# Optimization experiments

Hardware: AMD Instinct MI355X
Metric: run time of the kernel (lower is better)

Reference implementation:

```python
import jax, jax.numpy as jnp
import numpy as np

B, N, D, H = 64, 2048, 512, 512
CA, CB = 3, 5  # num classes per node type
EPS = 1e-5


def setup_inputs() -> dict:
    key = jax.random.key(0)
    ks = jax.random.split(key, 8)
    s = 1.0 / np.sqrt(D)
    x = jax.random.normal(ks[0], (B, N, D), dtype=jnp.float32)
    W1 = jax.random.uniform(ks[1], (D, H), jnp.float32, -s, s)
    b1 = jax.random.uniform(ks[2], (H,), jnp.float32, -s, s)
    gamma = jnp.ones((H,), jnp.float32)
    beta = jnp.zeros((H,), jnp.float32)
    sh = 1.0 / np.sqrt(H)
    Wa = jax.random.uniform(ks[3], (H, CA), jnp.float32, -sh, sh)
    ba = jax.random.uniform(ks[4], (CA,), jnp.float32, -sh, sh)
    Wb = jax.random.uniform(ks[5], (H, CB), jnp.float32, -sh, sh)
    bb = jax.random.uniform(ks[6], (CB,), jnp.float32, -sh, sh)
    idx_a = jnp.arange(0, N // 2, dtype=jnp.int64 if jax.config.jax_enable_x64 else jnp.int32)
    idx_b = jnp.arange(N // 2, N, dtype=idx_a.dtype)
    return {"x": x, "W1": W1, "b1": b1, "gamma": gamma, "beta": beta,
            "Wa": Wa, "ba": ba, "Wb": Wb, "bb": bb, "idx_a": idx_a, "idx_b": idx_b}


def reference(x, W1, b1, gamma, beta, Wa, ba, Wb, bb, idx_a, idx_b):
    # MLP block: Linear -> BatchNorm1d (training stats) -> ReLU on flattened rows
    h = x.reshape(-1, x.shape[-1]) @ W1 + b1            # [B*N, H]
    mu = h.mean(axis=0)
    var = h.var(axis=0)                                  # biased var, as BatchNorm1d normalization
    h = (h - mu) * jax.lax.rsqrt(var + EPS) * gamma + beta
    h = jax.nn.relu(h).reshape(x.shape[0], x.shape[1], -1)  # [B, N, H]

    out = jnp.zeros((x.shape[0], x.shape[1], 1), dtype=jnp.float32)
    for idx, W, b in ((idx_a, Wa, ba), (idx_b, Wb, bb)):
        logits = jnp.einsum('bnh,hc->bnc', h[:, idx, :], W) + b
        probs = jax.nn.softmax(logits, axis=-1)
        pred = jnp.argmax(probs, axis=-1, keepdims=True).astype(jnp.float32)
        out = out.at[:, idx, :].set(pred)
    return out
```

## Files before the change

kernel.cpp:

```cpp
#include <hip/hip_runtime.h>
#include <math.h>

constexpr int Bc = 64, Nc = 2048, Dc = 512, Hc = 512;
constexpr long long Mc = (long long)Bc * Nc;
constexpr int BM = 128, BN = 128, BK = 16;
constexpr int LDT = 132;

__global__ __launch_bounds__(256) void gemm_bias(const float* __restrict__ X,
                                                 const float* __restrict__ W,
                                                 const float* __restrict__ bias,
                                                 float* __restrict__ Hout)
{
    __shared__ float As[BK][LDT];
    __shared__ float Bs[BK][LDT];

    const int tid = threadIdx.x;
    const int bn = blockIdx.x;
    const int bm = blockIdx.y;
    const int m0 = bm * BM, n0 = bn * BN;

    const int wave = tid >> 6, lane = tid & 63;
    const int wm = wave >> 1, wn = wave & 1;
    const int lm = lane >> 3, ln = lane & 7;
    const int am = wm * 64 + lm * 8;
    const int an = wn * 64 + ln * 8;

    const int ar0 = tid >> 2;
    const int ak0 = (tid & 3) * 4;
    const int br0 = tid >> 5;
    const int bq0 = (tid & 31) * 4;

    const float* aBase = X + (size_t)(m0 + ar0) * Dc + ak0;
    const float* bBase = W + (size_t)br0 * Hc + n0 + bq0;

    float acc[8][8];
#pragma unroll
    for (int i = 0; i < 8; ++i)
#pragma unroll
        for (int j = 0; j < 8; ++j) acc[i][j] = 0.0f;

    float4 av0 = *(const float4*)(aBase);
    float4 av1 = *(const float4*)(aBase + (size_t)64 * Dc);
    float4 bv0 = *(const float4*)(bBase);
    float4 bv1 = *(const float4*)(bBase + (size_t)8 * Hc);

    for (int kt = 0; kt < Dc; kt += BK) {
        __syncthreads();
        As[ak0 + 0][ar0] = av0.x;  As[ak0 + 1][ar0] = av0.y;
        As[ak0 + 2][ar0] = av0.z;  As[ak0 + 3][ar0] = av0.w;
        As[ak0 + 0][ar0 + 64] = av1.x;  As[ak0 + 1][ar0 + 64] = av1.y;
        As[ak0 + 2][ar0 + 64] = av1.z;  As[ak0 + 3][ar0 + 64] = av1.w;
        *(float4*)&Bs[br0][bq0]     = bv0;
        *(float4*)&Bs[br0 + 8][bq0] = bv1;
        __syncthreads();

        const int kn = kt + BK;
        if (kn < Dc) {
            av0 = *(const float4*)(aBase + kn);
            av1 = *(const float4*)(aBase + (size_t)64 * Dc + kn);
            bv0 = *(const float4*)(bBase + (size_t)kn * Hc);
            bv1 = *(const float4*)(bBase + (size_t)(kn + 8) * Hc);
        }

#pragma unroll
        for (int k = 0; k < BK; ++k) {
            float4 a0 = *(const float4*)&As[k][am];
            float4 a1 = *(const float4*)&As[k][am + 4];
            float4 b0 = *(const float4*)&Bs[k][an];
            float4 b1 = *(const float4*)&Bs[k][an + 4];
            float a_[8] = {a0.x, a0.y, a0.z, a0.w, a1.x, a1.y, a1.z, a1.w};
            float b_[8] = {b0.x, b0.y, b0.z, b0.w, b1.x, b1.y, b1.z, b1.w};
#pragma unroll
            for (int i = 0; i < 8; ++i)
#pragma unroll
                for (int j = 0; j < 8; ++j)
                    acc[i][j] = fmaf(a_[i], b_[j], acc[i][j]);
        }
    }

    float4 c0 = *(const float4*)&bias[n0 + an];
    float4 c1 = *(const float4*)&bias[n0 + an + 4];
#pragma unroll
    for (int i = 0; i < 8; ++i) {
        const size_t row = (size_t)(m0 + am + i);
        float4 o0, o1;
        o0.x = acc[i][0] + c0.x; o0.y = acc[i][1] + c0.y;
        o0.z = acc[i][2] + c0.z; o0.w = acc[i][3] + c0.w;
        o1.x = acc[i][4] + c1.x; o1.y = acc[i][5] + c1.y;
        o1.z = acc[i][6] + c1.z; o1.w = acc[i][7] + c1.w;
        *(float4*)&Hout[row * Hc + n0 + an]     = o0;
        *(float4*)&Hout[row * Hc + n0 + an + 4] = o1;
    }
}

__global__ __launch_bounds__(256) void zero_stats(double* __restrict__ s)
{
    int i = blockIdx.x * 256 + threadIdx.x;
    if (i < 1024) s[i] = 0.0;
}

__global__ __launch_bounds__(256) void colstats(const float* __restrict__ Hbuf,
                                                double* __restrict__ sum,
                                                double* __restrict__ sumsq)
{
    const int c = threadIdx.x;
    const long long r0 = (long long)blockIdx.x * 256;
    float s0 = 0.f, q0 = 0.f, s1 = 0.f, q1 = 0.f;
    for (long long r = r0; r < r0 + 256; ++r) {
        float v0 = Hbuf[(size_t)r * Hc + c];
        float v1 = Hbuf[(size_t)r * Hc + c + 256];
        s0 += v0; q0 = fmaf(v0, v0, q0);
        s1 += v1; q1 = fmaf(v1, v1, q1);
    }
    atomicAdd(&sum[c], (double)s0);
    atomicAdd(&sumsq[c], (double)q0);
    atomicAdd(&sum[c + 256], (double)s1);
    atomicAdd(&sumsq[c + 256], (double)q1);
}

__global__ __launch_bounds__(256) void finalize_stats(const double* __restrict__ sum,
                                                      const double* __restrict__ sumsq,
                                                      const float* __restrict__ gamma,
                                                      const float* __restrict__ beta,
                                                      float* __restrict__ scale,
                                                      float* __restrict__ shift)
{
    int c = blockIdx.x * 256 + threadIdx.x;
    if (c < Hc) {
        double mu  = sum[c] / (double)Mc;
        double var = sumsq[c] / (double)Mc - mu * mu;
        double rstd = 1.0 / sqrt(var + 1e-5);
        float a = (float)rstd * gamma[c];
        scale[c] = a;
        shift[c] = beta[c] - (float)mu * a;
    }
}

template <int C>
__global__ __launch_bounds__(256) void head_kernel(const float* __restrict__ Hbuf,
                                                   const float* __restrict__ scale,
                                                   const float* __restrict__ shift,
                                                   const float* __restrict__ W,
                                                   const float* __restrict__ bias,
                                                   const int* __restrict__ idx,
                                                   float* __restrict__ out)
{
    const long long wid = ((long long)blockIdx.x * blockDim.x + threadIdx.x) >> 6;
    const int lane = threadIdx.x & 63;
    if (wid >= (long long)Bc * (Nc / 2)) return;
    const int b   = (int)(wid >> 10);
    const int pos = (int)(wid & 1023);
    const int n   = idx[pos];
    const size_t row = (size_t)b * Nc + n;

    const int i0 = lane * 8;
    float4 h0 = *(const float4*)&Hbuf[row * Hc + i0];
    float4 h1 = *(const float4*)&Hbuf[row * Hc + i0 + 4];
    float4 s0 = *(const float4*)&scale[i0];
    float4 s1 = *(const float4*)&scale[i0 + 4];
    float4 t0 = *(const float4*)&shift[i0];
    float4 t1 = *(const float4*)&shift[i0 + 4];

    float v[8];
    v[0] = fmaxf(fmaf(h0.x, s0.x, t0.x), 0.f);
    v[1] = fmaxf(fmaf(h0.y, s0.y, t0.y), 0.f);
    v[2] = fmaxf(fmaf(h0.z, s0.z, t0.z), 0.f);
    v[3] = fmaxf(fmaf(h0.w, s0.w, t0.w), 0.f);
    v[4] = fmaxf(fmaf(h1.x, s1.x, t1.x), 0.f);
    v[5] = fmaxf(fmaf(h1.y, s1.y, t1.y), 0.f);
    v[6] = fmaxf(fmaf(h1.z, s1.z, t1.z), 0.f);
    v[7] = fmaxf(fmaf(h1.w, s1.w, t1.w), 0.f);

    float p[C];
#pragma unroll
    for (int c = 0; c < C; ++c) p[c] = 0.f;
#pragma unroll
    for (int u = 0; u < 8; ++u) {
        const float* wrow = W + (size_t)(i0 + u) * C;
#pragma unroll
        for (int c = 0; c < C; ++c) p[c] = fmaf(v[u], wrow[c], p[c]);
    }
#pragma unroll
    for (int off = 32; off; off >>= 1)
#pragma unroll
        for (int c = 0; c < C; ++c) p[c] += __shfl_xor(p[c], off);

    if (lane == 0) {
        float best = p[0] + bias[0];
        int bi = 0;
#pragma unroll
        for (int c = 1; c < C; ++c) {
            float l = p[c] + bias[c];
            if (l > best) { best = l; bi = c; }
        }
        out[row] = (float)bi;
    }
}

extern "C" void kernel_launch(void* const* d_in, const int* in_sizes, int n_in,
                              void* d_out, int out_size, void* d_ws, size_t ws_size,
                              hipStream_t stream)
{
    (void)in_sizes; (void)n_in; (void)out_size; (void)ws_size;
    const float* x     = (const float*)d_in[0];
    const float* W1    = (const float*)d_in[1];
    const float* b1    = (const float*)d_in[2];
    const float* gamma = (const float*)d_in[3];
    const float* beta  = (const float*)d_in[4];
    const float* Wa    = (const float*)d_in[5];
    const float* ba    = (const float*)d_in[6];
    const float* Wb    = (const float*)d_in[7];
    const float* bb    = (const float*)d_in[8];
    const int*   idx_a = (const int*)d_in[9];
    const int*   idx_b = (const int*)d_in[10];
    float* out = (float*)d_out;

    char* ws = (char*)d_ws;
    float*  Hbuf  = (float*)ws;
    double* sums  = (double*)(ws + (size_t)Mc * Hc * 4);
    float*  scale = (float*)((char*)sums + 1024 * sizeof(double));
    float*  shift = scale + Hc;

    zero_stats<<<4, 256, 0, stream>>>(sums);
    gemm_bias<<<dim3(4, 1024), 256, 0, stream>>>(x, W1, b1, Hbuf);
    colstats<<<512, 256, 0, stream>>>(Hbuf, sums, sums + 512);
    finalize_stats<<<2, 256, 0, stream>>>(sums, sums + 512, gamma, beta, scale, shift);

    const long long waves_half = (long long)Bc * (Nc / 2);
    const int blocks_half = (int)((waves_half * 64 + 255) / 256);
    head_kernel<3><<<blocks_half, 256, 0, stream>>>(Hbuf, scale, shift, Wa, ba, idx_a, out);
    head_kernel<5><<<blocks_half, 256, 0, stream>>>(Hbuf, scale, shift, Wb, bb, idx_b, out);
}
```

Baseline: 1.154 ms.

## Fuse column stats into GEMM epilogue, async-load W to LDS, merge head kernels

Folds the BatchNorm column sum and sum-of-squares reduction into the GEMM epilogue using wave shuffles, shared memory and double atomics. This removes the separate colstats pass, which reread the whole 256 MB H buffer. The GEMM now uses BK=32, loads W tiles straight into double-buffered LDS with global_load_lds, and maps workgroups to XCDs to improve L2 locality. The two head kernels become one launch, which cuts launch overhead at the cost of more LDS use and a more complex GEMM schedule.

```diff
diff --git a/kernel.cpp b/kernel.cpp
--- a/kernel.cpp
+++ b/kernel.cpp
@@ -3,35 +3,56 @@
 
 constexpr int Bc = 64, Nc = 2048, Dc = 512, Hc = 512;
 constexpr long long Mc = (long long)Bc * Nc;
-constexpr int BM = 128, BN = 128, BK = 16;
-constexpr int LDT = 132;
-
-__global__ __launch_bounds__(256) void gemm_bias(const float* __restrict__ X,
-                                                 const float* __restrict__ W,
-                                                 const float* __restrict__ bias,
-                                                 float* __restrict__ Hout)
-{
-    __shared__ float As[BK][LDT];
-    __shared__ float Bs[BK][LDT];
+constexpr int BM = 128, BN = 128, BK = 32;
+constexpr int LDA_ = 132;
+
+__device__ __forceinline__ void gload16(const float* g, void* lds) {
+    __builtin_amdgcn_global_load_lds(
+        (const __attribute__((address_space(1))) void*)g,
+        (__attribute__((address_space(3))) void*)lds, 16, 0, 0);
+}
+
+__global__ __launch_bounds__(256) void gemm_fused(const float* __restrict__ X,
+                                                  const float* __restrict__ W,
+                                                  const float* __restrict__ bias,
+                                                  float* __restrict__ Hout,
+                                                  double* __restrict__ stats )
+{
+    __shared__ float As[BK][LDA_];
+    __shared__ float Bs[2][BK][BN];
+    __shared__ float sred[4][128];
+
+    const int wgid = blockIdx.x;
+    const int xcd  = wgid & 7;
+    const int slot = wgid >> 3;
+    const int bm   = xcd * 128 + (slot >> 2);
+    const int bn   = slot & 3;
+    const int m0 = bm * BM, n0 = bn * BN;
 
     const int tid = threadIdx.x;
-    const int bn = blockIdx.x;
-    const int bm = blockIdx.y;
-    const int m0 = bm * BM, n0 = bn * BN;
-
     const int wave = tid >> 6, lane = tid & 63;
     const int wm = wave >> 1, wn = wave & 1;
     const int lm = lane >> 3, ln = lane & 7;
     const int am = wm * 64 + lm * 8;
     const int an = wn * 64 + ln * 8;
 
-    const int ar0 = tid >> 2;
-    const int ak0 = (tid & 3) * 4;
-    const int br0 = tid >> 5;
-    const int bq0 = (tid & 31) * 4;
-
-    const float* aBase = X + (size_t)(m0 + ar0) * Dc + ak0;
-    const float* bBase = W + (size_t)br0 * Hc + n0 + bq0;
+    const int ar = tid >> 3;
+    const int ak = (tid & 7) << 2;
+    const float* aPtr = X + (size_t)(m0 + ar) * Dc + ak;
+
+    const int bkw = wave * 8 + (lane >> 5);
+    const int bc  = (lane & 31) << 2;
+    const float* wPtr = W + (size_t)bkw * Hc + n0 + bc;
+    char* bsBase = (char*)&Bs[0][0][0];
+
+#pragma unroll
+    for (int t = 0; t < 4; ++t) {
+        int off = __builtin_amdgcn_readfirstlane(wave * 4096 + t * 1024);
+        gload16(wPtr + (size_t)(2 * t) * Hc, bsBase + off);
+    }
+    float4 areg[4];
+#pragma unroll
+    for (int p = 0; p < 4; ++p) areg[p] = *(const float4*)(aPtr + (size_t)p * 32 * Dc);
 
     float acc[8][8];
 #pragma unroll
@@ -39,37 +60,35 @@
 #pragma unroll
         for (int j = 0; j < 8; ++j) acc[i][j] = 0.0f;
 
-    float4 av0 = *(const float4*)(aBase);
-    float4 av1 = *(const float4*)(aBase + (size_t)64 * Dc);
-    float4 bv0 = *(const float4*)(bBase);
-    float4 bv1 = *(const float4*)(bBase + (size_t)8 * Hc);
-
-    for (int kt = 0; kt < Dc; kt += BK) {
+    for (int it = 0; it < 16; ++it) {
+        const int cur = it & 1;
         __syncthreads();
-        As[ak0 + 0][ar0] = av0.x;  As[ak0 + 1][ar0] = av0.y;
-        As[ak0 + 2][ar0] = av0.z;  As[ak0 + 3][ar0] = av0.w;
-        As[ak0 + 0][ar0 + 64] = av1.x;  As[ak0 + 1][ar0 + 64] = av1.y;
-        As[ak0 + 2][ar0 + 64] = av1.z;  As[ak0 + 3][ar0 + 64] = av1.w;
-        *(float4*)&Bs[br0][bq0]     = bv0;
-        *(float4*)&Bs[br0 + 8][bq0] = bv1;
+#pragma unroll
+        for (int p = 0; p < 4; ++p) {
+            const int r = ar + 32 * p;
+            As[ak + 0][r] = areg[p].x;  As[ak + 1][r] = areg[p].y;
+            As[ak + 2][r] = areg[p].z;  As[ak + 3][r] = areg[p].w;
+        }
         __syncthreads();
-
-        const int kn = kt + BK;
-        if (kn < Dc) {
-            av0 = *(const float4*)(aBase + kn);
-            av1 = *(const float4*)(aBase + (size_t)64 * Dc + kn);
-            bv0 = *(const float4*)(bBase + (size_t)kn * Hc);
-            bv1 = *(const float4*)(bBase + (size_t)(kn + 8) * Hc);
-        }
-
-#pragma unroll
+        if (it < 15) {
+            const int ktn = (it + 1) * BK;
+#pragma unroll
+            for (int t = 0; t < 4; ++t) {
+                int off = __builtin_amdgcn_readfirstlane((cur ^ 1) * 16384 + wave * 4096 + t * 1024);
+                gload16(wPtr + (size_t)(ktn + 2 * t) * Hc, bsBase + off);
+            }
+#pragma unroll
+            for (int p = 0; p < 4; ++p)
+                areg[p] = *(const float4*)(aPtr + (size_t)p * 32 * Dc + ktn);
+        }
+        const float (*Bcur)[BN] = Bs[cur];
+#pragma unroll 8
         for (int k = 0; k < BK; ++k) {
-            float4 a0 = *(const float4*)&As[k][am];
-            float4 a1 = *(const float4*)&As[k][am + 4];
-            float4 b0 = *(const float4*)&Bs[k][an];
-            float4 b1 = *(const float4*)&Bs[k][an + 4];
-            float a_[8] = {a0.x, a0.y, a0.z, a0.w, a1.x, a1.y, a1.z, a1.w};
-            float b_[8] = {b0.x, b0.y, b0.z, b0.w, b1.x, b1.y, b1.z, b1.w};
+            const float* ap = &As[k][am];
+            const float* bp = &Bcur[k][an];
+            float a_[8], b_[8];
+#pragma unroll
+            for (int u = 0; u < 8; ++u) { a_[u] = ap[u]; b_[u] = bp[u]; }
 #pragma unroll
             for (int i = 0; i < 8; ++i)
 #pragma unroll
@@ -80,42 +99,53 @@
 
     float4 c0 = *(const float4*)&bias[n0 + an];
     float4 c1 = *(const float4*)&bias[n0 + an + 4];
+    float bz[8] = {c0.x, c0.y, c0.z, c0.w, c1.x, c1.y, c1.z, c1.w};
+    float s_[8], q_[8];
+#pragma unroll
+    for (int u = 0; u < 8; ++u) { s_[u] = 0.f; q_[u] = 0.f; }
 #pragma unroll
     for (int i = 0; i < 8; ++i) {
+        float v[8];
+#pragma unroll
+        for (int j = 0; j < 8; ++j) {
+            v[j] = acc[i][j] + bz[j];
+            s_[j] += v[j];
+            q_[j] = fmaf(v[j], v[j], q_[j]);
+        }
         const size_t row = (size_t)(m0 + am + i);
-        float4 o0, o1;
-        o0.x = acc[i][0] + c0.x; o0.y = acc[i][1] + c0.y;
-        o0.z = acc[i][2] + c0.z; o0.w = acc[i][3] + c0.w;
-        o1.x = acc[i][4] + c1.x; o1.y = acc[i][5] + c1.y;
-        o1.z = acc[i][6] + c1.z; o1.w = acc[i][7] + c1.w;
+        float4 o0 = {v[0], v[1], v[2], v[3]};
+        float4 o1 = {v[4], v[5], v[6], v[7]};
         *(float4*)&Hout[row * Hc + n0 + an]     = o0;
         *(float4*)&Hout[row * Hc + n0 + an + 4] = o1;
     }
+#pragma unroll
+    for (int off = 8; off < 64; off <<= 1) {
+#pragma unroll
+        for (int u = 0; u < 8; ++u) {
+            s_[u] += __shfl_xor(s_[u], off);
+            q_[u] += __shfl_xor(q_[u], off);
+        }
+    }
+    if (lm == 0) {
+#pragma unroll
+        for (int u = 0; u < 8; ++u) {
+            sred[wave][ln * 16 + u]     = s_[u];
+            sred[wave][ln * 16 + 8 + u] = q_[u];
+        }
+    }
+    __syncthreads();
+    {
+        const int wn2 = tid >> 7, ln2 = (tid >> 4) & 7, u = tid & 15;
+        float v = sred[wn2][ln2 * 16 + u] + sred[wn2 + 2][ln2 * 16 + u];
+        const int col = n0 + wn2 * 64 + ln2 * 8 + (u & 7);
+        atomicAdd(&stats[(u >> 3) * Hc + col], (double)v);
+    }
 }
 
 __global__ __launch_bounds__(256) void zero_stats(double* __restrict__ s)
 {
     int i = blockIdx.x * 256 + threadIdx.x;
     if (i < 1024) s[i] = 0.0;
-}
-
-__global__ __launch_bounds__(256) void colstats(const float* __restrict__ Hbuf,
-                                                double* __restrict__ sum,
-                                                double* __restrict__ sumsq)
-{
-    const int c = threadIdx.x;
-    const long long r0 = (long long)blockIdx.x * 256;
-    float s0 = 0.f, q0 = 0.f, s1 = 0.f, q1 = 0.f;
-    for (long long r = r0; r < r0 + 256; ++r) {
-        float v0 = Hbuf[(size_t)r * Hc + c];
-        float v1 = Hbuf[(size_t)r * Hc + c + 256];
-        s0 += v0; q0 = fmaf(v0, v0, q0);
-        s1 += v1; q1 = fmaf(v1, v1, q1);
-    }
-    atomicAdd(&sum[c], (double)s0);
-    atomicAdd(&sumsq[c], (double)q0);
-    atomicAdd(&sum[c + 256], (double)s1);
-    atomicAdd(&sumsq[c + 256], (double)q1);
 }
 
 __global__ __launch_bounds__(256) void finalize_stats(const double* __restrict__ sum,
@@ -137,20 +167,16 @@
 }
 
 template <int C>
-__global__ __launch_bounds__(256) void head_kernel(const float* __restrict__ Hbuf,
-                                                   const float* __restrict__ scale,
-                                                   const float* __restrict__ shift,
-                                                   const float* __restrict__ W,
-                                                   const float* __restrict__ bias,
-                                                   const int* __restrict__ idx,
-                                                   float* __restrict__ out)
-{
-    const long long wid = ((long long)blockIdx.x * blockDim.x + threadIdx.x) >> 6;
-    const int lane = threadIdx.x & 63;
-    if (wid >= (long long)Bc * (Nc / 2)) return;
-    const int b   = (int)(wid >> 10);
-    const int pos = (int)(wid & 1023);
-    const int n   = idx[pos];
+__device__ __forceinline__ void head_body(int hw, const int* __restrict__ idx,
+                                          const float* __restrict__ Wc,
+                                          const float* __restrict__ bc,
+                                          const float* __restrict__ Hbuf,
+                                          const float* __restrict__ scale,
+                                          const float* __restrict__ shift,
+                                          float* __restrict__ out, int lane)
+{
+    const int b = hw >> 10, pos = hw & 1023;
+    const int n = idx[pos];
     const size_t row = (size_t)b * Nc + n;
 
     const int i0 = lane * 8;
@@ -176,7 +202,7 @@
     for (int c = 0; c < C; ++c) p[c] = 0.f;
 #pragma unroll
     for (int u = 0; u < 8; ++u) {
-        const float* wrow = W + (size_t)(i0 + u) * C;
+        const float* wrow = Wc + (size_t)(i0 + u) * C;
 #pragma unroll
         for (int c = 0; c < C; ++c) p[c] = fmaf(v[u], wrow[c], p[c]);
     }
@@ -186,15 +212,34 @@
         for (int c = 0; c < C; ++c) p[c] += __shfl_xor(p[c], off);
 
     if (lane == 0) {
-        float best = p[0] + bias[0];
+        float best = p[0] + bc[0];
         int bi = 0;
 #pragma unroll
         for (int c = 1; c < C; ++c) {
-            float l = p[c] + bias[c];
+            float l = p[c] + bc[c];
             if (l > best) { best = l; bi = c; }
         }
         out[row] = (float)bi;
     }
+}
+
+__global__ __launch_bounds__(256) void heads_kernel(const float* __restrict__ Hbuf,
+                                                    const float* __restrict__ scale,
+                                                    const float* __restrict__ shift,
+                                                    const float* __restrict__ Wa,
+                                                    const float* __restrict__ ba,
+                                                    const int* __restrict__ idx_a,
+                                                    const float* __restrict__ Wb,
+                                                    const float* __restrict__ bb,
+                                                    const int* __restrict__ idx_b,
+                                                    float* __restrict__ out)
+{
+    const int wid = blockIdx.x * 4 + (threadIdx.x >> 6);
+    const int lane = threadIdx.x & 63;
+    if (wid < 65536)
+        head_body<3>(wid, idx_a, Wa, ba, Hbuf, scale, shift, out, lane);
+    else
+        head_body<5>(wid - 65536, idx_b, Wb, bb, Hbuf, scale, shift, out, lane);
 }
 
 extern "C" void kernel_launch(void* const* d_in, const int* in_sizes, int n_in,
@@ -217,17 +262,12 @@
 
     char* ws = (char*)d_ws;
     float*  Hbuf  = (float*)ws;
-    double* sums  = (double*)(ws + (size_t)Mc * Hc * 4);
-    float*  scale = (float*)((char*)sums + 1024 * sizeof(double));
+    double* stats = (double*)(ws + (size_t)Mc * Hc * 4);
+    float*  scale = (float*)((char*)stats + 1024 * sizeof(double));
     float*  shift = scale + Hc;
 
-    zero_stats<<<4, 256, 0, stream>>>(sums);
-    gemm_bias<<<dim3(4, 1024), 256, 0, stream>>>(x, W1, b1, Hbuf);
-    colstats<<<512, 256, 0, stream>>>(Hbuf, sums, sums + 512);
-    finalize_stats<<<2, 256, 0, stream>>>(sums, sums + 512, gamma, beta, scale, shift);
-
-    const long long waves_half = (long long)Bc * (Nc / 2);
-    const int blocks_half = (int)((waves_half * 64 + 255) / 256);
-    head_kernel<3><<<blocks_half, 256, 0, stream>>>(Hbuf, scale, shift, Wa, ba, idx_a, out);
-    head_kernel<5><<<blocks_half, 256, 0, stream>>>(Hbuf, scale, shift, Wb, bb, idx_b, out);
-}
+    zero_stats<<<4, 256, 0, stream>>>(stats);
+    gemm_fused<<<4096, 256, 0, stream>>>(x, W1, b1, Hbuf, stats);
+    finalize_stats<<<2, 256, 0, stream>>>(stats, stats + 512, gamma, beta, scale, shift);
+    heads_kernel<<<32768, 256, 0, stream>>>(Hbuf, scale, shift, Wa, ba, idx_a, Wb, bb, idx_b, out);
+}
```

After: 1.166 ms. About the same (+1.1%).
